# Kernel optimization log

Measured on AMD Instinct MI355X. Metric: run time of the kernel, lower is better.

Reference implementation:

```python
import jax, jax.numpy as jnp
import numpy as np

TEMPERATURE = 0.05   # distiller.temperature
KD_WEIGHT = 1.0      # args.kd_weight
EPS = 1e-8
B, D = 128, 768


def _huber(diff):
    a = jnp.abs(diff)
    return jnp.where(a < 1.0, 0.5 * a * a, a - 0.5)


def _pairwise_sqdist(x):
    # ||xi||^2 + ||xj||^2 - 2 xi.xj  (squared euclidean, as in source)
    n2 = (x * x).sum(axis=1, keepdims=True)
    return n2 + n2.T - 2.0 * (x @ x.T)


def _distance_loss(s, t):
    ds = _pairwise_sqdist(s)          # [N,N]
    dt = _pairwise_sqdist(t)
    n = ds.shape[0]
    mask = jnp.triu(jnp.ones((n, n), bool), k=1)
    cnt = n * (n - 1) / 2.0
    mean_sd = jax.lax.stop_gradient(jnp.where(mask, ds, 0.0).sum() / cnt) + EPS
    mean_td = jnp.where(mask, dt, 0.0).sum() / cnt + EPS  # teacher is constant anyway
    loss = _huber(ds / mean_sd - dt / mean_td)
    return jnp.where(mask, loss, 0.0).sum() / cnt


def _angle_potentials(x):
    # diffs[i,j] = x[j] - x[i]; unit vectors; cos[i,j,k] = e[i,j] . e[k,j]
    diffs = x[None, :, :] - x[:, None, :]                       # [N,N,D]
    e = diffs / (jnp.linalg.norm(diffs, axis=-1, keepdims=True) + EPS)
    return jnp.einsum('ijd,kjd->ijk', e, e)                     # [N,N,N]


def _angle_loss(s, t):
    ps = _angle_potentials(s)
    pt = _angle_potentials(t)
    n = ps.shape[0]
    i = jnp.arange(n)
    # valid iff i != j, i != k, j != k  (matches the three masked diagonals)
    m = ((i[:, None, None] != i[None, :, None]) &
         (i[:, None, None] != i[None, None, :]) &
         (i[None, :, None] != i[None, None, :]))
    cnt = n * (n - 1) * (n - 2)
    return jnp.where(m, _huber(ps - pt), 0.0).sum() / cnt


def _contrastive_loss(sq, sp):
    scores = (sq @ sp.T) / TEMPERATURE                          # [B,B]
    tgt = jnp.arange(scores.shape[0])                           # * (B//B) == arange
    logZ = jax.nn.logsumexp(scores, axis=-1)
    return (logZ - jnp.take_along_axis(scores, tgt[:, None], axis=1)[:, 0]).mean()


def setup_inputs() -> dict:
    key = jax.random.key(0)
    k1, k2, k3, k4 = jax.random.split(key, 4)
    return {
        'student_qry': jax.random.normal(k1, (B, D), jnp.float32),
        'student_pos': jax.random.normal(k2, (B, D), jnp.float32),
        'teacher_qry': jax.random.normal(k3, (B, D), jnp.float32),
        'teacher_pos': jax.random.normal(k4, (B, D), jnp.float32),
    }


def reference(student_qry, student_pos, teacher_qry, teacher_pos):
    contrastive = _contrastive_loss(student_qry, student_pos)
    s = jnp.concatenate([student_qry, student_pos], axis=0)     # [2B,D]
    t = jnp.concatenate([teacher_qry, teacher_pos], axis=0)
    t = jax.lax.stop_gradient(t)                                # teacher under no_grad
    kd = 0.5 * _distance_loss(s, t) + 0.5 * _angle_loss(s, t)
    total = contrastive + KD_WEIGHT * kd
    return total, contrastive, kd
```

## Files before the change

### kernel.cpp

```cpp
#include <hip/hip_runtime.h>
#include <math.h>

#define N2   256
#define DIM  768
#define EPSF 1e-8f

#define OFF_PART  0u
#define OFF_PDIAG 1048576u
#define OFF_TSUM  1052672u
#define OFF_GS    1052928u
#define OFF_GT    1118464u
#define OFF_INVS  1184000u
#define OFF_INVT  1249536u
#define OFF_SLOT  1315072u
#define SL_ANG  0
#define SL_DIST 512
#define SL_CON  768

__device__ inline float wave_reduce_sum(float v) {
    #pragma unroll
    for (int o = 32; o > 0; o >>= 1) v += __shfl_down(v, o, 64);
    return v;
}
__device__ inline float wave_reduce_max(float v) {
    #pragma unroll
    for (int o = 32; o > 0; o >>= 1) v = fmaxf(v, __shfl_down(v, o, 64));
    return v;
}
__device__ inline float block_reduce_sum(float v, volatile float* red) {
    float w = wave_reduce_sum(v);
    __syncthreads();
    if ((threadIdx.x & 63) == 0) red[threadIdx.x >> 6] = w;
    __syncthreads();
    return red[0] + red[1] + red[2] + red[3];
}
__device__ inline const float* rowptr(const float* q, const float* p, int r) {
    return (r < 128) ? (q + r * DIM) : (p + (r - 128) * DIM);
}

__global__ __launch_bounds__(256) void gemm_kernel(
        const float* __restrict__ sq, const float* __restrict__ sp,
        const float* __restrict__ tq, const float* __restrict__ tp,
        float* __restrict__ ws) {
    const int b = blockIdx.x, t = threadIdx.x;
    const int c = b & 7, mat = (b >> 3) & 1, tile = b >> 4;
    const int m0 = (tile >> 2) * 64, n0 = (tile & 3) * 64;
    const float* q = mat ? tq : sq;
    const float* p = mat ? tp : sp;

    __shared__ float As[64][100];
    __shared__ float Bs[64][100];
    __shared__ float redg[4];

    const int srow = t >> 2, skq = (t & 3) * 4;
    const int kb = c * 96;
    const float* arow = rowptr(q, p, m0 + srow);
    const float* brow = rowptr(q, p, n0 + srow);
    #pragma unroll
    for (int m = 0; m < 6; ++m) {
        *(float4*)&As[srow][skq + 16 * m] = *(const float4*)&arow[kb + skq + 16 * m];
        *(float4*)&Bs[srow][skq + 16 * m] = *(const float4*)&brow[kb + skq + 16 * m];
    }
    __syncthreads();

    const int ty = t >> 4, tx = t & 15;
    float acc[4][4] = {};
    for (int k = 0; k < 96; k += 4) {
        float4 av[4], bv[4];
        #pragma unroll
        for (int r = 0; r < 4; ++r) av[r] = *(const float4*)&As[ty + 16 * r][k];
        #pragma unroll
        for (int cc = 0; cc < 4; ++cc) bv[cc] = *(const float4*)&Bs[tx + 16 * cc][k];
        #pragma unroll
        for (int r = 0; r < 4; ++r) {
            const float ar4[4] = {av[r].x, av[r].y, av[r].z, av[r].w};
            #pragma unroll
            for (int cc = 0; cc < 4; ++cc) {
                const float bc4[4] = {bv[cc].x, bv[cc].y, bv[cc].z, bv[cc].w};
                acc[r][cc] = fmaf(ar4[0], bc4[0], acc[r][cc]);
                acc[r][cc] = fmaf(ar4[1], bc4[1], acc[r][cc]);
                acc[r][cc] = fmaf(ar4[2], bc4[2], acc[r][cc]);
                acc[r][cc] = fmaf(ar4[3], bc4[3], acc[r][cc]);
            }
        }
    }
    float* P = ws + OFF_PART + (unsigned)(c * 2 + mat) * 65536u;
    float ts = 0.f;
    #pragma unroll
    for (int r = 0; r < 4; ++r) {
        const int row = m0 + ty + 16 * r;
        #pragma unroll
        for (int cc = 0; cc < 4; ++cc) {
            P[row * 256 + n0 + tx + 16 * cc] = acc[r][cc];
            ts += acc[r][cc];
        }
    }
    if (m0 == n0 && ty == tx) {
        float* PD = ws + OFF_PDIAG + (unsigned)(c * 2 + mat) * 256u;
        #pragma unroll
        for (int r = 0; r < 4; ++r) PD[m0 + ty + 16 * r] = acc[r][r];
    }
    const float tsum = block_reduce_sum(ts, redg);
    if (t == 0) ws[OFF_TSUM + (unsigned)(mat * 128 + c * 16 + tile)] = tsum;
}

__global__ __launch_bounds__(256) void prep_kernel(float* __restrict__ ws) {
    __shared__ float red1[4], red2[4], redS[1];
    const int i = blockIdx.x, j = threadIdx.x, t = threadIdx.x;

    const float* P  = ws + OFF_PART;
    const float* PD = ws + OFF_PDIAG;
    float gs = 0.f, gt = 0.f, djs = 0.f, djt = 0.f, dis = 0.f, dit = 0.f;
    #pragma unroll
    for (int c = 0; c < 8; ++c) {
        gs  += P[c * 131072 + i * 256 + j];
        gt  += P[c * 131072 + 65536 + i * 256 + j];
        djs += PD[c * 512 + j];
        djt += PD[c * 512 + 256 + j];
        dis += PD[c * 512 + i];
        dit += PD[c * 512 + 256 + i];
    }
    (ws + OFF_GS)[i * 256 + j] = gs;
    (ws + OFF_GT)[i * 256 + j] = gt;
    const float ds = fmaxf(dis + djs - 2.f * gs, 0.f);
    const float dt = fmaxf(dit + djt - 2.f * gt, 0.f);
    (ws + OFF_INVS)[i * 256 + j] = 1.f / (sqrtf(ds) + EPSF);
    (ws + OFF_INVT)[i * 256 + j] = 1.f / (sqrtf(dt) + EPSF);

    const float tr_s = block_reduce_sum(djs, red1);
    const float tr_t = block_reduce_sum(djt, red1);
    const float tv = ws[OFF_TSUM + t];
    const float sum_gs = block_reduce_sum((t < 128) ? tv : 0.f, red1);
    const float sum_gt = block_reduce_sum((t >= 128) ? tv : 0.f, red1);
    const float rs = 1.f / ((256.f * tr_s - sum_gs) / 32640.f + EPSF);
    const float rt = 1.f / ((256.f * tr_t - sum_gt) / 32640.f + EPSF);

    const float dd = ds * rs - dt * rt;
    const float a = fabsf(dd);
    const float m = fminf(a, 1.f);
    const float hv = block_reduce_sum((j > i) ? m * fmaf(-0.5f, m, a) : 0.f, red1);
    if (t == 0) ws[OFF_SLOT + SL_DIST + i] = hv;

    if (i < 128) {
        const float s = (j >= 128) ? 20.f * gs : -INFINITY;
        if (j == 128 + i) redS[0] = s;
        float mx0 = wave_reduce_max(s);
        __syncthreads();
        if ((t & 63) == 0) red2[t >> 6] = mx0;
        __syncthreads();
        const float mx = fmaxf(fmaxf(red2[0], red2[1]), fmaxf(red2[2], red2[3]));
        const float e = block_reduce_sum((j >= 128) ? expf(s - mx) : 0.f, red1);
        if (t == 0) ws[OFF_SLOT + SL_CON + i] = mx + logf(e) - redS[0];
    }
}

__global__ __launch_bounds__(256) void angle_kernel(float* __restrict__ ws) {
    const float* Gs = ws + OFF_GS;
    const float* Gt = ws + OFF_GT;
    const float* IS = ws + OFF_INVS;
    const float* IT = ws + OFF_INVT;
    __shared__ float sGJ[16][68], sIJ[16][68], sTJ[16][68], sITJ[16][68];
    __shared__ float red1[4];
    const int b = blockIdx.x, t = threadIdx.x;

    const int k0 = (b & 3) * 64;
    const int j0 = ((b >> 2) & 15) * 16;
    const int i0 = (b >> 6) * 32;
    const int jj = t & 15, ii = t >> 4;
    const int i1 = i0 + ii, i2 = i1 + 16, j = j0 + jj;
    {
        const int r = t >> 4, c = (t & 15) * 4;
        const int g = (j0 + r) * N2 + k0 + c;
        *(float4*)&sGJ[r][c]  = *(const float4*)&Gs[g];
        *(float4*)&sIJ[r][c]  = *(const float4*)&IS[g];
        *(float4*)&sTJ[r][c]  = *(const float4*)&Gt[g];
        *(float4*)&sITJ[r][c] = *(const float4*)&IT[g];
    }
    const float Gjj = Gs[j * 257], Tjj = Gt[j * 257];
    const float wis1 = IS[i1 * N2 + j], wit1 = IT[i1 * N2 + j];
    const float wis2 = IS[i2 * N2 + j], wit2 = IT[i2 * N2 + j];
    const float as1 = (Gjj - Gs[i1 * N2 + j]) * wis1;
    const float at1 = (Tjj - Gt[i1 * N2 + j]) * wit1;
    const float as2 = (Gjj - Gs[i2 * N2 + j]) * wis2;
    const float at2 = (Tjj - Gt[i2 * N2 + j]) * wit2;
    const float* gI1 = Gs + i1 * N2 + k0;
    const float* tI1 = Gt + i1 * N2 + k0;
    const float* gI2 = Gs + i2 * N2 + k0;
    const float* tI2 = Gt + i2 * N2 + k0;
    __syncthreads();

    float sum1 = 0.f, sum2 = 0.f;
    for (int c = 0; c < 64; c += 4) {
        const float4 gJ  = *(const float4*)&sGJ[jj][c];
        const float4 iJ  = *(const float4*)&sIJ[jj][c];
        const float4 tJ  = *(const float4*)&sTJ[jj][c];
        const float4 itJ = *(const float4*)&sITJ[jj][c];
        const float4 a1 = *(const float4*)&gI1[c];
        const float4 b1 = *(const float4*)&tI1[c];
        const float4 a2 = *(const float4*)&gI2[c];
        const float4 b2 = *(const float4*)&tI2[c];
        const float gJr[4]  = {gJ.x, gJ.y, gJ.z, gJ.w};
        const float iJr[4]  = {iJ.x, iJ.y, iJ.z, iJ.w};
        const float tJr[4]  = {tJ.x, tJ.y, tJ.z, tJ.w};
        const float itJr[4] = {itJ.x, itJ.y, itJ.z, itJ.w};
        const float a1r[4] = {a1.x, a1.y, a1.z, a1.w};
        const float b1r[4] = {b1.x, b1.y, b1.z, b1.w};
        const float a2r[4] = {a2.x, a2.y, a2.z, a2.w};
        const float b2r[4] = {b2.x, b2.y, b2.z, b2.w};
        #pragma unroll
        for (int e = 0; e < 4; ++e) {
            const float ps1 = fmaf(wis1, a1r[e] - gJr[e], as1) * iJr[e];
            const float pt1 = fmaf(wit1, b1r[e] - tJr[e], at1) * itJr[e];
            const float d1 = ps1 - pt1;
            const float ad1 = fabsf(d1);
            const float m1 = fminf(ad1, 1.f);
            sum1 = fmaf(m1, fmaf(-0.5f, m1, ad1), sum1);

            const float ps2 = fmaf(wis2, a2r[e] - gJr[e], as2) * iJr[e];
            const float pt2 = fmaf(wit2, b2r[e] - tJr[e], at2) * itJr[e];
            const float d2 = ps2 - pt2;
            const float ad2 = fabsf(d2);
            const float m2 = fminf(ad2, 1.f);
            sum2 = fmaf(m2, fmaf(-0.5f, m2, ad2), sum2);
        }
    }
    const float v = block_reduce_sum(sum1 + sum2, red1);
    if (t == 0) ws[OFF_SLOT + SL_ANG + b] = v;
}

__global__ __launch_bounds__(256) void finalize_kernel(const float* __restrict__ ws,
                                                       float* __restrict__ out) {
    __shared__ float red1[4];
    const int t = threadIdx.x;
    const float* S = ws + OFF_SLOT;
    const float a_ = block_reduce_sum(S[SL_ANG + t] + S[SL_ANG + 256 + t], red1);
    const float d_ = block_reduce_sum(S[SL_DIST + t], red1);
    const float c_ = block_reduce_sum((t < 128) ? S[SL_CON + t] : 0.f, red1);
    if (t == 0) {
        const float contrastive = c_ / 128.f;
        const float dist = d_ / 32640.f;
        const float ang = a_ / 16581120.f;
        const float kd = 0.5f * (dist + ang);
        out[0] = contrastive + kd;
        out[1] = contrastive;
        out[2] = kd;
    }
}

extern "C" void kernel_launch(void* const* d_in, const int* in_sizes, int n_in,
                              void* d_out, int out_size, void* d_ws, size_t ws_size,
                              hipStream_t stream) {
    (void)in_sizes; (void)n_in; (void)out_size; (void)ws_size;
    const float* sq = (const float*)d_in[0];
    const float* sp = (const float*)d_in[1];
    const float* tq = (const float*)d_in[2];
    const float* tp = (const float*)d_in[3];
    float* ws  = (float*)d_ws;
    float* out = (float*)d_out;

    gemm_kernel<<<256, 256, 0, stream>>>(sq, sp, tq, tp, ws);
    prep_kernel<<<256, 256, 0, stream>>>(ws);
    angle_kernel<<<512, 256, 0, stream>>>(ws);
    finalize_kernel<<<1, 256, 0, stream>>>(ws, out);
}
```

Before: 84.17 us.

## Fuse prep and angle kernels, recomputing Gram sums and inverse norms per block

Merges the prep and angle kernels into one launch of 896 blocks. Angle blocks reduce the split-K Gram partials themselves and compute the inverse distances on the fly, removing the materialised Gs/Gt/inverse buffers and one kernel boundary. Distance and contrastive rows run as extra blocks in the same grid. In exchange, each angle block re-reads eight partial slices for its tiles, which adds redundant global traffic and reciprocal/sqrt work, and raises shared memory use per block.

```diff
diff --git a/kernel.cpp b/kernel.cpp
--- a/kernel.cpp
+++ b/kernel.cpp
@@ -8,11 +8,7 @@
 #define OFF_PART  0u
 #define OFF_PDIAG 1048576u
 #define OFF_TSUM  1052672u
-#define OFF_GS    1052928u
-#define OFF_GT    1118464u
-#define OFF_INVS  1184000u
-#define OFF_INVT  1249536u
-#define OFF_SLOT  1315072u
+#define OFF_SLOT  1052928u
 #define SL_ANG  0
 #define SL_DIST 512
 #define SL_CON  768
@@ -104,128 +100,181 @@
     if (t == 0) ws[OFF_TSUM + (unsigned)(mat * 128 + c * 16 + tile)] = tsum;
 }
 
-__global__ __launch_bounds__(256) void prep_kernel(float* __restrict__ ws) {
-    __shared__ float red1[4], red2[4], redS[1];
-    const int i = blockIdx.x, j = threadIdx.x, t = threadIdx.x;
-
+__global__ __launch_bounds__(256) void mega_kernel(float* __restrict__ ws) {
     const float* P  = ws + OFF_PART;
     const float* PD = ws + OFF_PDIAG;
-    float gs = 0.f, gt = 0.f, djs = 0.f, djt = 0.f, dis = 0.f, dit = 0.f;
-    #pragma unroll
-    for (int c = 0; c < 8; ++c) {
-        gs  += P[c * 131072 + i * 256 + j];
-        gt  += P[c * 131072 + 65536 + i * 256 + j];
-        djs += PD[c * 512 + j];
-        djt += PD[c * 512 + 256 + j];
-        dis += PD[c * 512 + i];
-        dit += PD[c * 512 + 256 + i];
-    }
-    (ws + OFF_GS)[i * 256 + j] = gs;
-    (ws + OFF_GT)[i * 256 + j] = gt;
-    const float ds = fmaxf(dis + djs - 2.f * gs, 0.f);
-    const float dt = fmaxf(dit + djt - 2.f * gt, 0.f);
-    (ws + OFF_INVS)[i * 256 + j] = 1.f / (sqrtf(ds) + EPSF);
-    (ws + OFF_INVT)[i * 256 + j] = 1.f / (sqrtf(dt) + EPSF);
-
-    const float tr_s = block_reduce_sum(djs, red1);
-    const float tr_t = block_reduce_sum(djt, red1);
-    const float tv = ws[OFF_TSUM + t];
-    const float sum_gs = block_reduce_sum((t < 128) ? tv : 0.f, red1);
-    const float sum_gt = block_reduce_sum((t >= 128) ? tv : 0.f, red1);
-    const float rs = 1.f / ((256.f * tr_s - sum_gs) / 32640.f + EPSF);
-    const float rt = 1.f / ((256.f * tr_t - sum_gt) / 32640.f + EPSF);
-
-    const float dd = ds * rs - dt * rt;
-    const float a = fabsf(dd);
-    const float m = fminf(a, 1.f);
-    const float hv = block_reduce_sum((j > i) ? m * fmaf(-0.5f, m, a) : 0.f, red1);
-    if (t == 0) ws[OFF_SLOT + SL_DIST + i] = hv;
-
-    if (i < 128) {
+    __shared__ float sGJ[16][68], sTJ[16][68], sIJ[16][68], sITJ[16][68];
+    __shared__ float sGI[32][68], sTI[32][68];
+    __shared__ float dgS[256], dgT[256];
+    __shared__ float red1[4], red2[4], redS[1];
+    const int b = blockIdx.x, t = threadIdx.x;
+
+    if (b < 512) {
+        const int k0 = (b & 3) * 64;
+        const int j0 = ((b >> 2) & 15) * 16;
+        const int i0 = (b >> 6) * 32;
+        const int jj = t & 15, ii = t >> 4;
+        const int i1 = i0 + ii, i2 = i1 + 16, j = j0 + jj;
+
+        {
+            float as = 0.f, at_ = 0.f;
+            #pragma unroll
+            for (int c = 0; c < 8; ++c) {
+                as  += PD[c * 512 + t];
+                at_ += PD[c * 512 + 256 + t];
+            }
+            dgS[t] = as; dgT[t] = at_;
+        }
+        const int r = t >> 4, c4 = (t & 15) * 4;
+        float4 gjs = {0,0,0,0}, gjt = {0,0,0,0};
+        {
+            const unsigned base = (unsigned)((j0 + r) * 256 + k0 + c4);
+            #pragma unroll
+            for (int c = 0; c < 8; ++c) {
+                const float4 a = *(const float4*)&P[c * 131072u + base];
+                const float4 e = *(const float4*)&P[c * 131072u + 65536u + base];
+                gjs.x += a.x; gjs.y += a.y; gjs.z += a.z; gjs.w += a.w;
+                gjt.x += e.x; gjt.y += e.y; gjt.z += e.z; gjt.w += e.w;
+            }
+        }
+        #pragma unroll
+        for (int s2 = 0; s2 < 2; ++s2) {
+            const int slot = t + 256 * s2;
+            const int ri = slot >> 4, ci = (slot & 15) * 4;
+            const unsigned base = (unsigned)((i0 + ri) * 256 + k0 + ci);
+            float4 gs = {0,0,0,0}, gt = {0,0,0,0};
+            #pragma unroll
+            for (int c = 0; c < 8; ++c) {
+                const float4 a = *(const float4*)&P[c * 131072u + base];
+                const float4 e = *(const float4*)&P[c * 131072u + 65536u + base];
+                gs.x += a.x; gs.y += a.y; gs.z += a.z; gs.w += a.w;
+                gt.x += e.x; gt.y += e.y; gt.z += e.z; gt.w += e.w;
+            }
+            *(float4*)&sGI[ri][ci] = gs;
+            *(float4*)&sTI[ri][ci] = gt;
+        }
+        float g1s = 0.f, g1t = 0.f, g2s = 0.f, g2t = 0.f;
+        #pragma unroll
+        for (int c = 0; c < 8; ++c) {
+            g1s += P[c * 131072u + (unsigned)(i1 * 256 + j)];
+            g1t += P[c * 131072u + 65536u + (unsigned)(i1 * 256 + j)];
+            g2s += P[c * 131072u + (unsigned)(i2 * 256 + j)];
+            g2t += P[c * 131072u + 65536u + (unsigned)(i2 * 256 + j)];
+        }
+        __syncthreads();
+
+        {
+            const float djs = dgS[j0 + r], djt = dgT[j0 + r];
+            float4 ivs, ivt;
+            const float* dS = &dgS[k0 + c4];
+            const float* dT = &dgT[k0 + c4];
+            ivs.x = 1.f / (sqrtf(fmaxf(djs + dS[0] - 2.f * gjs.x, 0.f)) + EPSF);
+            ivs.y = 1.f / (sqrtf(fmaxf(djs + dS[1] - 2.f * gjs.y, 0.f)) + EPSF);
+            ivs.z = 1.f / (sqrtf(fmaxf(djs + dS[2] - 2.f * gjs.z, 0.f)) + EPSF);
+            ivs.w = 1.f / (sqrtf(fmaxf(djs + dS[3] - 2.f * gjs.w, 0.f)) + EPSF);
+            ivt.x = 1.f / (sqrtf(fmaxf(djt + dT[0] - 2.f * gjt.x, 0.f)) + EPSF);
+            ivt.y = 1.f / (sqrtf(fmaxf(djt + dT[1] - 2.f * gjt.y, 0.f)) + EPSF);
+            ivt.z = 1.f / (sqrtf(fmaxf(djt + dT[2] - 2.f * gjt.z, 0.f)) + EPSF);
+            ivt.w = 1.f / (sqrtf(fmaxf(djt + dT[3] - 2.f * gjt.w, 0.f)) + EPSF);
+            *(float4*)&sGJ[r][c4] = gjs;
+            *(float4*)&sTJ[r][c4] = gjt;
+            *(float4*)&sIJ[r][c4] = ivs;
+            *(float4*)&sITJ[r][c4] = ivt;
+        }
+        const float Gjj = dgS[j], Tjj = dgT[j];
+        const float wis1 = 1.f / (sqrtf(fmaxf(dgS[i1] + Gjj - 2.f * g1s, 0.f)) + EPSF);
+        const float wit1 = 1.f / (sqrtf(fmaxf(dgT[i1] + Tjj - 2.f * g1t, 0.f)) + EPSF);
+        const float wis2 = 1.f / (sqrtf(fmaxf(dgS[i2] + Gjj - 2.f * g2s, 0.f)) + EPSF);
+        const float wit2 = 1.f / (sqrtf(fmaxf(dgT[i2] + Tjj - 2.f * g2t, 0.f)) + EPSF);
+        const float as1 = (Gjj - g1s) * wis1;
+        const float at1 = (Tjj - g1t) * wit1;
+        const float as2 = (Gjj - g2s) * wis2;
+        const float at2 = (Tjj - g2t) * wit2;
+        __syncthreads();
+
+        float sum1 = 0.f, sum2 = 0.f;
+        for (int c = 0; c < 64; c += 4) {
+            const float4 gJ  = *(const float4*)&sGJ[jj][c];
+            const float4 iJ  = *(const float4*)&sIJ[jj][c];
+            const float4 tJ  = *(const float4*)&sTJ[jj][c];
+            const float4 itJ = *(const float4*)&sITJ[jj][c];
+            const float4 a1 = *(const float4*)&sGI[ii][c];
+            const float4 b1 = *(const float4*)&sTI[ii][c];
+            const float4 a2 = *(const float4*)&sGI[ii + 16][c];
+            const float4 b2 = *(const float4*)&sTI[ii + 16][c];
+            const float gJr[4]  = {gJ.x, gJ.y, gJ.z, gJ.w};
+            const float iJr[4]  = {iJ.x, iJ.y, iJ.z, iJ.w};
+            const float tJr[4]  = {tJ.x, tJ.y, tJ.z, tJ.w};
+            const float itJr[4] = {itJ.x, itJ.y, itJ.z, itJ.w};
+            const float a1r[4] = {a1.x, a1.y, a1.z, a1.w};
+            const float b1r[4] = {b1.x, b1.y, b1.z, b1.w};
+            const float a2r[4] = {a2.x, a2.y, a2.z, a2.w};
+            const float b2r[4] = {b2.x, b2.y, b2.z, b2.w};
+            #pragma unroll
+            for (int e = 0; e < 4; ++e) {
+                const float ps1 = fmaf(wis1, a1r[e] - gJr[e], as1) * iJr[e];
+                const float pt1 = fmaf(wit1, b1r[e] - tJr[e], at1) * itJr[e];
+                const float d1 = ps1 - pt1;
+                const float ad1 = fabsf(d1);
+                const float m1 = fminf(ad1, 1.f);
+                sum1 = fmaf(m1, fmaf(-0.5f, m1, ad1), sum1);
+
+                const float ps2 = fmaf(wis2, a2r[e] - gJr[e], as2) * iJr[e];
+                const float pt2 = fmaf(wit2, b2r[e] - tJr[e], at2) * itJr[e];
+                const float d2 = ps2 - pt2;
+                const float ad2 = fabsf(d2);
+                const float m2 = fminf(ad2, 1.f);
+                sum2 = fmaf(m2, fmaf(-0.5f, m2, ad2), sum2);
+            }
+        }
+        const float v = block_reduce_sum(sum1 + sum2, red1);
+        if (t == 0) ws[OFF_SLOT + SL_ANG + b] = v;
+    } else if (b < 768) {
+        const int i = b - 512, j = t;
+        float gs = 0.f, gt = 0.f, djs = 0.f, djt = 0.f, dis = 0.f, dit = 0.f;
+        #pragma unroll
+        for (int c = 0; c < 8; ++c) {
+            gs  += P[c * 131072u + (unsigned)(i * 256 + j)];
+            gt  += P[c * 131072u + 65536u + (unsigned)(i * 256 + j)];
+            djs += PD[c * 512 + j];
+            djt += PD[c * 512 + 256 + j];
+            dis += PD[c * 512 + i];
+            dit += PD[c * 512 + 256 + i];
+        }
+        const float ds = fmaxf(dis + djs - 2.f * gs, 0.f);
+        const float dt = fmaxf(dit + djt - 2.f * gt, 0.f);
+
+        const float tr_s = block_reduce_sum(djs, red1);
+        const float tr_t = block_reduce_sum(djt, red1);
+        const float tv = ws[OFF_TSUM + t];
+        const float sum_gs = block_reduce_sum((t < 128) ? tv : 0.f, red1);
+        const float sum_gt = block_reduce_sum((t >= 128) ? tv : 0.f, red1);
+        const float rs = 1.f / ((256.f * tr_s - sum_gs) / 32640.f + EPSF);
+        const float rt = 1.f / ((256.f * tr_t - sum_gt) / 32640.f + EPSF);
+
+        const float dd = ds * rs - dt * rt;
+        const float a = fabsf(dd);
+        const float m = fminf(a, 1.f);
+        const float hv = block_reduce_sum((j > i) ? m * fmaf(-0.5f, m, a) : 0.f, red1);
+        if (t == 0) ws[OFF_SLOT + SL_DIST + i] = hv;
+    } else {
+        const int rrow = b - 768, j = t;
+        float gs = 0.f;
+        if (j >= 128) {
+            #pragma unroll
+            for (int c = 0; c < 8; ++c)
+                gs += P[c * 131072u + (unsigned)(rrow * 256 + j)];
+        }
         const float s = (j >= 128) ? 20.f * gs : -INFINITY;
-        if (j == 128 + i) redS[0] = s;
+        if (j == 128 + rrow) redS[0] = s;
         float mx0 = wave_reduce_max(s);
         __syncthreads();
         if ((t & 63) == 0) red2[t >> 6] = mx0;
         __syncthreads();
         const float mx = fmaxf(fmaxf(red2[0], red2[1]), fmaxf(red2[2], red2[3]));
         const float e = block_reduce_sum((j >= 128) ? expf(s - mx) : 0.f, red1);
-        if (t == 0) ws[OFF_SLOT + SL_CON + i] = mx + logf(e) - redS[0];
-    }
-}
-
-__global__ __launch_bounds__(256) void angle_kernel(float* __restrict__ ws) {
-    const float* Gs = ws + OFF_GS;
-    const float* Gt = ws + OFF_GT;
-    const float* IS = ws + OFF_INVS;
-    const float* IT = ws + OFF_INVT;
-    __shared__ float sGJ[16][68], sIJ[16][68], sTJ[16][68], sITJ[16][68];
-    __shared__ float red1[4];
-    const int b = blockIdx.x, t = threadIdx.x;
-
-    const int k0 = (b & 3) * 64;
-    const int j0 = ((b >> 2) & 15) * 16;
-    const int i0 = (b >> 6) * 32;
-    const int jj = t & 15, ii = t >> 4;
-    const int i1 = i0 + ii, i2 = i1 + 16, j = j0 + jj;
-    {
-        const int r = t >> 4, c = (t & 15) * 4;
-        const int g = (j0 + r) * N2 + k0 + c;
-        *(float4*)&sGJ[r][c]  = *(const float4*)&Gs[g];
-        *(float4*)&sIJ[r][c]  = *(const float4*)&IS[g];
-        *(float4*)&sTJ[r][c]  = *(const float4*)&Gt[g];
-        *(float4*)&sITJ[r][c] = *(const float4*)&IT[g];
-    }
-    const float Gjj = Gs[j * 257], Tjj = Gt[j * 257];
-    const float wis1 = IS[i1 * N2 + j], wit1 = IT[i1 * N2 + j];
-    const float wis2 = IS[i2 * N2 + j], wit2 = IT[i2 * N2 + j];
-    const float as1 = (Gjj - Gs[i1 * N2 + j]) * wis1;
-    const float at1 = (Tjj - Gt[i1 * N2 + j]) * wit1;
-    const float as2 = (Gjj - Gs[i2 * N2 + j]) * wis2;
-    const float at2 = (Tjj - Gt[i2 * N2 + j]) * wit2;
-    const float* gI1 = Gs + i1 * N2 + k0;
-    const float* tI1 = Gt + i1 * N2 + k0;
-    const float* gI2 = Gs + i2 * N2 + k0;
-    const float* tI2 = Gt + i2 * N2 + k0;
-    __syncthreads();
-
-    float sum1 = 0.f, sum2 = 0.f;
-    for (int c = 0; c < 64; c += 4) {
-        const float4 gJ  = *(const float4*)&sGJ[jj][c];
-        const float4 iJ  = *(const float4*)&sIJ[jj][c];
-        const float4 tJ  = *(const float4*)&sTJ[jj][c];
-        const float4 itJ = *(const float4*)&sITJ[jj][c];
-        const float4 a1 = *(const float4*)&gI1[c];
-        const float4 b1 = *(const float4*)&tI1[c];
-        const float4 a2 = *(const float4*)&gI2[c];
-        const float4 b2 = *(const float4*)&tI2[c];
-        const float gJr[4]  = {gJ.x, gJ.y, gJ.z, gJ.w};
-        const float iJr[4]  = {iJ.x, iJ.y, iJ.z, iJ.w};
-        const float tJr[4]  = {tJ.x, tJ.y, tJ.z, tJ.w};
-        const float itJr[4] = {itJ.x, itJ.y, itJ.z, itJ.w};
-        const float a1r[4] = {a1.x, a1.y, a1.z, a1.w};
-        const float b1r[4] = {b1.x, b1.y, b1.z, b1.w};
-        const float a2r[4] = {a2.x, a2.y, a2.z, a2.w};
-        const float b2r[4] = {b2.x, b2.y, b2.z, b2.w};
-        #pragma unroll
-        for (int e = 0; e < 4; ++e) {
-            const float ps1 = fmaf(wis1, a1r[e] - gJr[e], as1) * iJr[e];
-            const float pt1 = fmaf(wit1, b1r[e] - tJr[e], at1) * itJr[e];
-            const float d1 = ps1 - pt1;
-            const float ad1 = fabsf(d1);
-            const float m1 = fminf(ad1, 1.f);
-            sum1 = fmaf(m1, fmaf(-0.5f, m1, ad1), sum1);
-
-            const float ps2 = fmaf(wis2, a2r[e] - gJr[e], as2) * iJr[e];
-            const float pt2 = fmaf(wit2, b2r[e] - tJr[e], at2) * itJr[e];
-            const float d2 = ps2 - pt2;
-            const float ad2 = fabsf(d2);
-            const float m2 = fminf(ad2, 1.f);
-            sum2 = fmaf(m2, fmaf(-0.5f, m2, ad2), sum2);
-        }
-    }
-    const float v = block_reduce_sum(sum1 + sum2, red1);
-    if (t == 0) ws[OFF_SLOT + SL_ANG + b] = v;
+        if (t == 0) ws[OFF_SLOT + SL_CON + rrow] = mx + logf(e) - redS[0];
+    }
 }
 
 __global__ __launch_bounds__(256) void finalize_kernel(const float* __restrict__ ws,
@@ -259,7 +308,6 @@
     float* out = (float*)d_out;
 
     gemm_kernel<<<256, 256, 0, stream>>>(sq, sp, tq, tp, ws);
-    prep_kernel<<<256, 256, 0, stream>>>(ws);
-    angle_kernel<<<512, 256, 0, stream>>>(ws);
+    mega_kernel<<<896, 256, 0, stream>>>(ws);
     finalize_kernel<<<1, 256, 0, stream>>>(ws, out);
 }
```

New measurement: 83.59 us. No clear change (-0.7%).
